# Performance work log

Measured on AMD Instinct MI355X. Metric: run time of the kernel, lower is better.

The kernel has to match this reference:

```python
import jax, jax.numpy as jnp
import numpy as np

N = 10000      # nodes
E = 320000     # edges
F_IN = 33      # input node features
H = 32         # hidden
G = 64         # graphs in batch


def setup_inputs() -> dict:
    key = jax.random.key(0)
    ks = jax.random.split(key, 24)
    s = 0.1  # small init scale for numerical sanity
    inp = {
        "x": jax.random.normal(ks[0], (N, F_IN), jnp.float32),
        "edge_index": jax.random.randint(ks[1], (2, E), 0, N, jnp.int32),
        "edge_attr": jax.random.uniform(ks[2], (E, 1), jnp.float32),
        "batch": jnp.sort(jax.random.randint(ks[3], (N,), 0, G, jnp.int32)),
        # conv1: edge-MLP Linear(1 -> F_IN*H), root weight [F_IN,H], bias [H]
        "nn_w1": jax.random.normal(ks[4], (1, F_IN * H), jnp.float32) * s,
        "nn_b1": jax.random.normal(ks[5], (F_IN * H,), jnp.float32) * s,
        "root1": jax.random.normal(ks[6], (F_IN, H), jnp.float32) * s,
        "bias1": jnp.zeros((H,), jnp.float32),
        # conv2: edge-MLP Linear(1 -> H*H)
        "nn_w2": jax.random.normal(ks[7], (1, H * H), jnp.float32) * s,
        "nn_b2": jax.random.normal(ks[8], (H * H,), jnp.float32) * s,
        "root2": jax.random.normal(ks[9], (H, H), jnp.float32) * s,
        "bias2": jnp.zeros((H,), jnp.float32),
        # conv3
        "nn_w3": jax.random.normal(ks[10], (1, H * H), jnp.float32) * s,
        "nn_b3": jax.random.normal(ks[11], (H * H,), jnp.float32) * s,
        "root3": jax.random.normal(ks[12], (H, H), jnp.float32) * s,
        "bias3": jnp.zeros((H,), jnp.float32),
        # readout MLP: Linear(3H -> H), Linear(H -> 2)
        "lin1_w": jax.random.normal(ks[13], (3 * H, H), jnp.float32) * s,
        "lin1_b": jnp.zeros((H,), jnp.float32),
        "lin2_w": jax.random.normal(ks[14], (H, 2), jnp.float32) * s,
        "lin2_b": jnp.zeros((2,), jnp.float32),
    }
    return inp


def _nnconv(x, src, dst, edge_attr, nn_w, nn_b, root, bias):
    """PyG NNConv (aggr='add'): out_i = x_i @ root + bias + sum_{e: dst(e)=i} x_{src(e)} @ Theta(e_attr)."""
    in_dim, out_dim = root.shape
    # per-edge weight matrix from edge MLP: [E, in, out]
    W = (edge_attr @ nn_w + nn_b).reshape(-1, in_dim, out_dim)
    msg = jnp.einsum('ei,eio->eo', x[src], W)          # gather + per-edge small matmul
    agg = jax.ops.segment_sum(msg, dst, num_segments=N)  # scatter-add into targets
    return agg + x @ root + bias


def reference(x, edge_index, edge_attr, batch,
              nn_w1, nn_b1, root1, bias1,
              nn_w2, nn_b2, root2, bias2,
              nn_w3, nn_b3, root3, bias3,
              lin1_w, lin1_b, lin2_w, lin2_b):
    src, dst = edge_index[0], edge_index[1]
    h = jax.nn.relu(_nnconv(x, src, dst, edge_attr, nn_w1, nn_b1, root1, bias1))
    h = jax.nn.relu(_nnconv(h, src, dst, edge_attr, nn_w2, nn_b2, root2, bias2))
    h = jax.nn.relu(_nnconv(h, src, dst, edge_attr, nn_w3, nn_b3, root3, bias3))
    # global add / mean / max pooling over graphs
    add_p = jax.ops.segment_sum(h, batch, num_segments=G)
    cnt = jax.ops.segment_sum(jnp.ones((N, 1), h.dtype), batch, num_segments=G)
    mean_p = add_p / jnp.maximum(cnt, 1.0)
    max_p = jax.ops.segment_max(h, batch, num_segments=G)
    max_p = jnp.where(jnp.isfinite(max_p), max_p, 0.0)  # guard empty segments
    g = jnp.concatenate([add_p, mean_p, max_p], axis=1)  # [G, 3H]
    g = jax.nn.relu(g @ lin1_w + lin1_b)
    # dropout p=0.5 is identity in eval mode
    logits = g @ lin2_w + lin2_b
    return jax.nn.log_softmax(logits, axis=-1)
```

## Files before the change

### kernel.cpp

```cpp
#include <hip/hip_runtime.h>

constexpr int N_  = 10000;
constexpr int E_  = 320000;
constexpr int F1  = 33;
constexpr int H   = 32;
constexpr int G   = 64;
constexpr int CAP = 96;
constexpr int NB_ = 1280;
constexpr int ROW = CAP * 8;

constexpr int EBLK = E_ / 256;
constexpr int PBLK = N_ / 8;
constexpr int SLICES = 32;
constexpr int CHUNKS = 16;
constexpr int TILE   = 640;
constexpr int AT    = 1024;
constexpr int ITERS = TILE / 128;

__device__ __forceinline__ unsigned bf16r(float x) {
    unsigned u = __float_as_uint(x);
    return (u + 0x7FFFu + ((u >> 16) & 1u)) >> 16;
}

__device__ __forceinline__ size_t mslot(int n, int pos) {
    return (size_t)(n >> 3) * ROW + (size_t)(pos >> 3) * 64 + (n & 7) * 8 + (pos & 7);
}


__global__ __launch_bounds__(256) void k_build_pre1(
        const int* __restrict__ ei, const float* __restrict__ ea,
        const float* __restrict__ x, const int* __restrict__ batch,
        const float* __restrict__ A, const float* __restrict__ Bm,
        const float* __restrict__ Rw, const float* __restrict__ bias,
        int* __restrict__ counts, unsigned* __restrict__ meta2,
        unsigned* __restrict__ UVs, float* __restrict__ Rs,
        int* __restrict__ startsP) {
    __shared__ unsigned s_uv[32][9];
    __shared__ float    s_r[32][9];
    if (blockIdx.x < EBLK) {
        int e = blockIdx.x * 256 + threadIdx.x;
        int s = ei[e];
        int d = ei[E_ + e];
        int pos = atomicAdd(&counts[d], 1);
        meta2[mslot(d, pos)] = (unsigned)s | (bf16r(ea[e]) << 16);
    } else {
        int base8 = (blockIdx.x - EBLK) * 8;
        int grp = threadIdx.x >> 5;
        int f = threadIdx.x & 31;
        int node = base8 + grp;
        if (f == 0) {
            int b = batch[node];
            int bp = (node == 0) ? -1 : batch[node - 1];
            if (b != bp) startsP[b] = node + 1;
        }
        float u = 0.f, v = 0.f, r = bias[f];
        const float* xr = x + (size_t)node * F1;
        #pragma unroll
        for (int k = 0; k < F1; ++k) {
            float xv = xr[k];
            u = fmaf(xv, A[k * H + f], u);
            v = fmaf(xv, Bm[k * H + f], v);
            r = fmaf(xv, Rw[k * H + f], r);
        }
        s_uv[f][grp] = bf16r(u) | (bf16r(v) << 16);
        s_r[f][grp]  = r;
        __syncthreads();
        int fo = threadIdx.x >> 3;
        int nl = threadIdx.x & 7;
        UVs[(size_t)fo * N_ + base8 + nl] = s_uv[fo][nl];
        Rs [(size_t)fo * N_ + base8 + nl] = s_r [fo][nl];
    }
}


__global__ __launch_bounds__(256) void k_pre(
        const float* __restrict__ Hs,
        const float* __restrict__ A, const float* __restrict__ Bm,
        const float* __restrict__ Rw, const float* __restrict__ bias,
        unsigned* __restrict__ UVs, float* __restrict__ Rs) {
    __shared__ unsigned s_uv[32][9];
    __shared__ float    s_r[32][9];
    int base8 = blockIdx.x * 8;
    int grp = threadIdx.x >> 5;
    int f = threadIdx.x & 31;
    int node = base8 + grp;
    float hv = Hs[(size_t)f * N_ + node];
    float u = 0.f, v = 0.f, r = bias[f];
    #pragma unroll
    for (int k = 0; k < H; ++k) {
        float hk = __shfl(hv, k, 32);
        u = fmaf(hk, A[k * H + f], u);
        v = fmaf(hk, Bm[k * H + f], v);
        r = fmaf(hk, Rw[k * H + f], r);
    }
    s_uv[f][grp] = bf16r(u) | (bf16r(v) << 16);
    s_r[f][grp]  = r;
    __syncthreads();
    int fo = threadIdx.x >> 3;
    int nl = threadIdx.x & 7;
    UVs[(size_t)fo * N_ + base8 + nl] = s_uv[fo][nl];
    Rs [(size_t)fo * N_ + base8 + nl] = s_r [fo][nl];
}


__global__ __launch_bounds__(1024, 8) void k_agg_lds(
        const int* __restrict__ counts, const unsigned* __restrict__ meta2,
        const unsigned* __restrict__ UVs, const float* __restrict__ Rs,
        float* __restrict__ Hs) {
    __shared__ __align__(16) unsigned uvl[N_];
    int s     = blockIdx.x & 31;
    int chunk = blockIdx.x >> 5;

    int l   = threadIdx.x & 63;
    int wav = threadIdx.x >> 6;
    int j0  = l & 7;
    int nl  = l >> 3;

    int cbase = chunk * TILE + wav * 8;
    int node = cbase + nl;
    int nc = min(node, N_ - 1);
    int dg = (node < N_) ? counts[nc] : 0;
    float rv = Rs[(size_t)s * N_ + nc];
    const unsigned* mrow = meta2 + (size_t)(cbase >> 3) * ROW + l;
    unsigned m0 = mrow[0], m1 = mrow[64], m2 = mrow[128],
             m3 = mrow[192], m4 = mrow[256], m5 = mrow[320];

    const unsigned* srcp = UVs + (size_t)s * N_;
    #pragma unroll
    for (int i = 0; i < 3; ++i) {
        int d4 = (i * AT + (int)threadIdx.x) * 4;
        if (d4 + 4 <= N_) {
            uint4 t = *reinterpret_cast<const uint4*>(srcp + d4);
            *reinterpret_cast<uint4*>(&uvl[d4]) = t;
        }
    }
    __syncthreads();

    for (int it = 0; it < ITERS; ++it) {
        int nbase = cbase + 128;
        int nnode = nbase + nl;
        int nnc = min(nnode, N_ - 1);
        int ndg = 0; float nrv = 0.f;
        unsigned n0 = 0, n1 = 0, n2 = 0, n3 = 0, n4 = 0, n5 = 0;
        if (it < ITERS - 1) {
            ndg = (nnode < N_) ? counts[nnc] : 0;
            nrv = Rs[(size_t)s * N_ + nnc];
            const unsigned* nmr = meta2 + (size_t)(nbase >> 3) * ROW + l;
            n0 = nmr[0]; n1 = nmr[64]; n2 = nmr[128];
            n3 = nmr[192]; n4 = nmr[256]; n5 = nmr[320];
        }

        float acc = 0.f;
        auto slot = [&](int p, unsigned mv) {
            unsigned idx = min(mv & 0xFFFFu, (unsigned)(N_ - 1));
            unsigned w = uvl[idx];
            float t = fmaf(__uint_as_float(mv & 0xFFFF0000u),
                           __uint_as_float(w << 16),
                           __uint_as_float(w & 0xFFFF0000u));
            if (j0 + 8 * p < dg) acc += t;
        };
        slot(0, m0); slot(1, m1); slot(2, m2);
        slot(3, m3); slot(4, m4); slot(5, m5);
        if (__any(dg > 48)) {
            const unsigned* trow = meta2 + (size_t)(cbase >> 3) * ROW + l;
            for (int p = 6; __any(j0 + 8 * p < dg); ++p)
                slot(p, trow[p * 64]);
        }
        acc += __shfl_xor(acc, 1);
        acc += __shfl_xor(acc, 2);
        acc += __shfl_xor(acc, 4);
        float h = fmaxf(rv + acc, 0.f);
        if (j0 == 0 && node < N_) Hs[(size_t)s * N_ + node] = h;

        cbase = nbase; node = nnode; nc = nnc; dg = ndg; rv = nrv;
        m0 = n0; m1 = n1; m2 = n2; m3 = n3; m4 = n4; m5 = n5;
    }
}


__global__ __launch_bounds__(256) void k_pool(
        const float* __restrict__ Hs, const int* __restrict__ startsP,
        const float* __restrict__ w1, const float* __restrict__ b1,
        const float* __restrict__ w2, const float* __restrict__ b2,
        float* __restrict__ out) {
    __shared__ int sst[G];
    __shared__ float ga[32], gm[32], gx[32];
    int tid = threadIdx.x;
    if (tid < G) sst[tid] = startsP[tid];
    __syncthreads();
    int g = blockIdx.x;
    int sp = sst[g];
    int s = 0, e = 0;
    if (sp != 0) {
        s = sp - 1;
        e = N_;
        for (int j = g + 1; j < G; ++j)
            if (sst[j]) { e = sst[j] - 1; break; }
    }
    int f = tid >> 3, oct = tid & 7;
    float sum = 0.f, mx = 0.f;
    for (int n = s + oct; n < e; n += 8) {
        float w = Hs[(size_t)f * N_ + n];
        sum += w;
        mx = fmaxf(mx, w);
    }
    sum += __shfl_xor(sum, 1); mx = fmaxf(mx, __shfl_xor(mx, 1));
    sum += __shfl_xor(sum, 2); mx = fmaxf(mx, __shfl_xor(mx, 2));
    sum += __shfl_xor(sum, 4); mx = fmaxf(mx, __shfl_xor(mx, 4));
    if (oct == 0) {
        float c = fmaxf((float)(e - s), 1.0f);
        ga[f] = sum;
        gm[f] = sum / c;
        gx[f] = mx;
    }
    __syncthreads();
    if (tid < 32) {
        float hacc = b1[tid];
        #pragma unroll
        for (int k = 0; k < H; ++k) {
            hacc = fmaf(ga[k], w1[k * H + tid], hacc);
            hacc = fmaf(gm[k], w1[(H + k) * H + tid], hacc);
            hacc = fmaf(gx[k], w1[(2 * H + k) * H + tid], hacc);
        }
        float hid = fmaxf(hacc, 0.f);
        float p0 = hid * w2[tid * 2 + 0];
        float p1 = hid * w2[tid * 2 + 1];
        #pragma unroll
        for (int offq = 16; offq; offq >>= 1) {
            p0 += __shfl_xor(p0, offq, 32);
            p1 += __shfl_xor(p1, offq, 32);
        }
        if (tid == 0) {
            float l0 = p0 + b2[0], l1 = p1 + b2[1];
            float m = fmaxf(l0, l1);
            float lse = m + logf(expf(l0 - m) + expf(l1 - m));
            out[g * 2 + 0] = l0 - lse;
            out[g * 2 + 1] = l1 - lse;
        }
    }
}


extern "C" void kernel_launch(void* const* d_in, const int* in_sizes, int n_in,
                              void* d_out, int out_size, void* d_ws, size_t ws_size,
                              hipStream_t stream) {
    const float* x      = (const float*)d_in[0];
    const int*   ei     = (const int*)  d_in[1];
    const float* ea     = (const float*)d_in[2];
    const int*   batch  = (const int*)  d_in[3];
    const float* nn_w1  = (const float*)d_in[4];
    const float* nn_b1  = (const float*)d_in[5];
    const float* root1  = (const float*)d_in[6];
    const float* bias1  = (const float*)d_in[7];
    const float* nn_w2  = (const float*)d_in[8];
    const float* nn_b2  = (const float*)d_in[9];
    const float* root2  = (const float*)d_in[10];
    const float* bias2  = (const float*)d_in[11];
    const float* nn_w3  = (const float*)d_in[12];
    const float* nn_b3  = (const float*)d_in[13];
    const float* root3  = (const float*)d_in[14];
    const float* bias3  = (const float*)d_in[15];
    const float* lin1_w = (const float*)d_in[16];
    const float* lin1_b = (const float*)d_in[17];
    const float* lin2_w = (const float*)d_in[18];
    const float* lin2_b = (const float*)d_in[19];
    float* out = (float*)d_out;

    char* ws = (char*)d_ws;
    size_t off = 0;
    auto alloc = [&](size_t bytes) -> void* {
        void* p = ws + off;
        off += (bytes + 255) & ~(size_t)255;
        return p;
    };
    const size_t zbytes = N_ * sizeof(int) + G * sizeof(int);
    char* zchunk = (char*)alloc(zbytes);
    int*  counts  = (int*)zchunk;
    int*  startsP = (int*)(zchunk + N_ * sizeof(int));
    unsigned* meta2 = (unsigned*)alloc((size_t)NB_ * ROW * sizeof(unsigned));
    unsigned* UVs1 = (unsigned*)alloc((size_t)H * N_ * sizeof(unsigned));
    unsigned* UVs2 = (unsigned*)alloc((size_t)H * N_ * sizeof(unsigned));
    unsigned* UVs3 = (unsigned*)alloc((size_t)H * N_ * sizeof(unsigned));
    float* Rs1 = (float*)alloc((size_t)H * N_ * sizeof(float));
    float* Rs2 = (float*)alloc((size_t)H * N_ * sizeof(float));
    float* Rs3 = (float*)alloc((size_t)H * N_ * sizeof(float));
    float* h1  = (float*)alloc((size_t)H * N_ * sizeof(float));
    float* h2  = (float*)alloc((size_t)H * N_ * sizeof(float));
    float* h3  = (float*)alloc((size_t)H * N_ * sizeof(float));

    hipMemsetAsync(zchunk, 0, zbytes, stream);

    k_build_pre1<<<EBLK + PBLK, 256, 0, stream>>>(ei, ea, x, batch,
                                                  nn_w1, nn_b1, root1, bias1,
                                                  counts, meta2, UVs1, Rs1, startsP);

    k_agg_lds<<<SLICES * CHUNKS, AT, 0, stream>>>(counts, meta2, UVs1, Rs1, h1);
    k_pre    <<<PBLK, 256, 0, stream>>>(h1, nn_w2, nn_b2, root2, bias2, UVs2, Rs2);
    k_agg_lds<<<SLICES * CHUNKS, AT, 0, stream>>>(counts, meta2, UVs2, Rs2, h2);
    k_pre    <<<PBLK, 256, 0, stream>>>(h2, nn_w3, nn_b3, root3, bias3, UVs3, Rs3);
    k_agg_lds<<<SLICES * CHUNKS, AT, 0, stream>>>(counts, meta2, UVs3, Rs3, h3);

    k_pool<<<G, 256, 0, stream>>>(h3, startsP, lin1_w, lin1_b, lin2_w, lin2_b, out);
}
```

Baseline: 169.3 us.

## Fuse all GNN stages into one persistent cooperative kernel with grid syncs

Replaces the memset plus seven separate launches with a single cooperative kernel of 256 blocks of 1024 threads. Grid-wide syncs separate the edge-bucketing, pre-transform, three aggregation and pooling phases, and the counter zeroing moves into the kernel. The aim is to remove launch gaps and tail effects between the small kernels. The cost is fewer blocks per aggregation pass (each block handles two chunks), a reshaped pre/pool work split, grid.sync overheads, and a multi-kernel fallback path if the cooperative launch fails.

```diff
diff --git a/kernel.cpp b/kernel.cpp
--- a/kernel.cpp
+++ b/kernel.cpp
@@ -1,4 +1,7 @@
 #include <hip/hip_runtime.h>
+#include <hip/hip_cooperative_groups.h>
+
+namespace cg = cooperative_groups;
 
 constexpr int N_  = 10000;
 constexpr int E_  = 320000;
@@ -9,13 +12,13 @@
 constexpr int NB_ = 1280;
 constexpr int ROW = CAP * 8;
 
-constexpr int EBLK = E_ / 256;
-constexpr int PBLK = N_ / 8;
+constexpr int GRID   = 256;
+constexpr int BT     = 1024;
 constexpr int SLICES = 32;
 constexpr int CHUNKS = 16;
 constexpr int TILE   = 640;
-constexpr int AT    = 1024;
-constexpr int ITERS = TILE / 128;
+constexpr int ITERS  = TILE / 128;
+constexpr int NG     = 2 * ITERS;
 
 __device__ __forceinline__ unsigned bf16r(float x) {
     unsigned u = __float_as_uint(x);
@@ -26,218 +29,278 @@
     return (size_t)(n >> 3) * ROW + (size_t)(pos >> 3) * 64 + (n & 7) * 8 + (pos & 7);
 }
 
-
-__global__ __launch_bounds__(256) void k_build_pre1(
-        const int* __restrict__ ei, const float* __restrict__ ea,
-        const float* __restrict__ x, const int* __restrict__ batch,
-        const float* __restrict__ A, const float* __restrict__ Bm,
-        const float* __restrict__ Rw, const float* __restrict__ bias,
-        int* __restrict__ counts, unsigned* __restrict__ meta2,
-        unsigned* __restrict__ UVs, float* __restrict__ Rs,
-        int* __restrict__ startsP) {
-    __shared__ unsigned s_uv[32][9];
-    __shared__ float    s_r[32][9];
-    if (blockIdx.x < EBLK) {
-        int e = blockIdx.x * 256 + threadIdx.x;
-        int s = ei[e];
-        int d = ei[E_ + e];
-        int pos = atomicAdd(&counts[d], 1);
-        meta2[mslot(d, pos)] = (unsigned)s | (bf16r(ea[e]) << 16);
-    } else {
-        int base8 = (blockIdx.x - EBLK) * 8;
-        int grp = threadIdx.x >> 5;
-        int f = threadIdx.x & 31;
-        int node = base8 + grp;
-        if (f == 0) {
-            int b = batch[node];
-            int bp = (node == 0) ? -1 : batch[node - 1];
-            if (b != bp) startsP[b] = node + 1;
-        }
-        float u = 0.f, v = 0.f, r = bias[f];
-        const float* xr = x + (size_t)node * F1;
+struct Prm {
+    const float* x; const int* ei; const float* ea; const int* batch;
+    const float* A1; const float* B1; const float* R1; const float* z1;
+    const float* A2; const float* B2; const float* R2; const float* z2;
+    const float* A3; const float* B3; const float* R3; const float* z3;
+    const float* l1w; const float* l1b; const float* l2w; const float* l2b;
+    int* counts; int* startsP; unsigned* meta2;
+    unsigned* UV; float* Rs; float* Hs;
+    float* out;
+};
+
+
+__device__ __forceinline__ void build_phase(const Prm& p, unsigned* uvl) {
+    const int tid = threadIdx.x;
+    const int bid = blockIdx.x;
+
+    for (int e = bid * BT + tid; e < E_; e += GRID * BT) {
+        int s = p.ei[e];
+        int d = p.ei[E_ + e];
+        int pos = atomicAdd(&p.counts[d], 1);
+        p.meta2[mslot(d, pos)] = (unsigned)s | (bf16r(p.ea[e]) << 16);
+    }
+
+    unsigned (*s_uv)[33] = reinterpret_cast<unsigned (*)[33]>(uvl);
+    float    (*s_r )[33] = reinterpret_cast<float (*)[33]>((float*)(uvl + 32 * 33));
+    int grp = tid >> 5, f = tid & 31;
+    for (int t = bid; t * 32 < N_; t += GRID) {
+        int node = t * 32 + grp;
+        int nc = min(node, N_ - 1);
+        if (f == 0 && node < N_) {
+            int b = p.batch[nc];
+            int bp = (node == 0) ? -1 : p.batch[nc - 1];
+            if (b != bp) p.startsP[b] = node + 1;
+        }
+        float u = 0.f, v = 0.f, r = p.z1[f];
+        const float* xr = p.x + (size_t)nc * F1;
         #pragma unroll
         for (int k = 0; k < F1; ++k) {
             float xv = xr[k];
-            u = fmaf(xv, A[k * H + f], u);
-            v = fmaf(xv, Bm[k * H + f], v);
-            r = fmaf(xv, Rw[k * H + f], r);
+            u = fmaf(xv, p.A1[k * H + f], u);
+            v = fmaf(xv, p.B1[k * H + f], v);
+            r = fmaf(xv, p.R1[k * H + f], r);
         }
         s_uv[f][grp] = bf16r(u) | (bf16r(v) << 16);
-        s_r[f][grp]  = r;
+        s_r [f][grp] = r;
         __syncthreads();
-        int fo = threadIdx.x >> 3;
-        int nl = threadIdx.x & 7;
-        UVs[(size_t)fo * N_ + base8 + nl] = s_uv[fo][nl];
-        Rs [(size_t)fo * N_ + base8 + nl] = s_r [fo][nl];
-    }
-}
-
-
-__global__ __launch_bounds__(256) void k_pre(
-        const float* __restrict__ Hs,
+        int fo = tid >> 5, nl = tid & 31;
+        int on = t * 32 + nl;
+        if (on < N_) {
+            p.UV[(size_t)fo * N_ + on] = s_uv[fo][nl];
+            p.Rs[(size_t)fo * N_ + on] = s_r [fo][nl];
+        }
+        __syncthreads();
+    }
+}
+
+
+__device__ __forceinline__ void pre_phase(const Prm& p, unsigned* uvl,
         const float* __restrict__ A, const float* __restrict__ Bm,
-        const float* __restrict__ Rw, const float* __restrict__ bias,
-        unsigned* __restrict__ UVs, float* __restrict__ Rs) {
-    __shared__ unsigned s_uv[32][9];
-    __shared__ float    s_r[32][9];
-    int base8 = blockIdx.x * 8;
-    int grp = threadIdx.x >> 5;
-    int f = threadIdx.x & 31;
-    int node = base8 + grp;
-    float hv = Hs[(size_t)f * N_ + node];
-    float u = 0.f, v = 0.f, r = bias[f];
-    #pragma unroll
-    for (int k = 0; k < H; ++k) {
-        float hk = __shfl(hv, k, 32);
-        u = fmaf(hk, A[k * H + f], u);
-        v = fmaf(hk, Bm[k * H + f], v);
-        r = fmaf(hk, Rw[k * H + f], r);
-    }
-    s_uv[f][grp] = bf16r(u) | (bf16r(v) << 16);
-    s_r[f][grp]  = r;
-    __syncthreads();
-    int fo = threadIdx.x >> 3;
-    int nl = threadIdx.x & 7;
-    UVs[(size_t)fo * N_ + base8 + nl] = s_uv[fo][nl];
-    Rs [(size_t)fo * N_ + base8 + nl] = s_r [fo][nl];
-}
-
-
-__global__ __launch_bounds__(1024, 8) void k_agg_lds(
-        const int* __restrict__ counts, const unsigned* __restrict__ meta2,
-        const unsigned* __restrict__ UVs, const float* __restrict__ Rs,
-        float* __restrict__ Hs) {
-    __shared__ __align__(16) unsigned uvl[N_];
-    int s     = blockIdx.x & 31;
-    int chunk = blockIdx.x >> 5;
-
-    int l   = threadIdx.x & 63;
-    int wav = threadIdx.x >> 6;
-    int j0  = l & 7;
-    int nl  = l >> 3;
-
-    int cbase = chunk * TILE + wav * 8;
+        const float* __restrict__ Rw, const float* __restrict__ bz) {
+    const int tid = threadIdx.x;
+    unsigned (*s_uv)[33] = reinterpret_cast<unsigned (*)[33]>(uvl);
+    float    (*s_r )[33] = reinterpret_cast<float (*)[33]>((float*)(uvl + 32 * 33));
+    int grp = tid >> 5, f = tid & 31;
+    for (int t = blockIdx.x; t * 32 < N_; t += GRID) {
+        int node = t * 32 + grp;
+        int nc = min(node, N_ - 1);
+        float hv = p.Hs[(size_t)f * N_ + nc];
+        float u = 0.f, v = 0.f, r = bz[f];
+        #pragma unroll
+        for (int k = 0; k < H; ++k) {
+            float hk = __shfl(hv, k, 32);
+            u = fmaf(hk, A[k * H + f], u);
+            v = fmaf(hk, Bm[k * H + f], v);
+            r = fmaf(hk, Rw[k * H + f], r);
+        }
+        s_uv[f][grp] = bf16r(u) | (bf16r(v) << 16);
+        s_r [f][grp] = r;
+        __syncthreads();
+        int fo = tid >> 5, nl = tid & 31;
+        int on = t * 32 + nl;
+        if (on < N_) {
+            p.UV[(size_t)fo * N_ + on] = s_uv[fo][nl];
+            p.Rs[(size_t)fo * N_ + on] = s_r [fo][nl];
+        }
+        __syncthreads();
+    }
+}
+
+
+__device__ __forceinline__ void agg_phase(const Prm& p, unsigned* uvl) {
+    const int tid = threadIdx.x;
+    const int s  = blockIdx.x & 31;
+    const int c0 = blockIdx.x >> 5;
+    const int l = tid & 63, wav = tid >> 6, j0 = l & 7, nl = l >> 3;
+
+    auto base_of = [&](int g) {
+        int ch = c0 + ((g >= ITERS) ? 8 : 0);
+        int it = (g >= ITERS) ? (g - ITERS) : g;
+        return ch * TILE + it * 128 + wav * 8;
+    };
+
+    int cbase = base_of(0);
     int node = cbase + nl;
     int nc = min(node, N_ - 1);
-    int dg = (node < N_) ? counts[nc] : 0;
-    float rv = Rs[(size_t)s * N_ + nc];
-    const unsigned* mrow = meta2 + (size_t)(cbase >> 3) * ROW + l;
+    int dg = (node < N_) ? p.counts[nc] : 0;
+    float rv = p.Rs[(size_t)s * N_ + nc];
+    const unsigned* mrow = p.meta2 + (size_t)(cbase >> 3) * ROW + l;
     unsigned m0 = mrow[0], m1 = mrow[64], m2 = mrow[128],
              m3 = mrow[192], m4 = mrow[256], m5 = mrow[320];
 
-    const unsigned* srcp = UVs + (size_t)s * N_;
+    const unsigned* srcp = p.UV + (size_t)s * N_;
     #pragma unroll
     for (int i = 0; i < 3; ++i) {
-        int d4 = (i * AT + (int)threadIdx.x) * 4;
-        if (d4 + 4 <= N_) {
-            uint4 t = *reinterpret_cast<const uint4*>(srcp + d4);
-            *reinterpret_cast<uint4*>(&uvl[d4]) = t;
-        }
+        int d4 = (i * BT + tid) * 4;
+        if (d4 + 4 <= N_)
+            *reinterpret_cast<uint4*>(&uvl[d4]) =
+                *reinterpret_cast<const uint4*>(srcp + d4);
     }
     __syncthreads();
 
-    for (int it = 0; it < ITERS; ++it) {
-        int nbase = cbase + 128;
-        int nnode = nbase + nl;
-        int nnc = min(nnode, N_ - 1);
-        int ndg = 0; float nrv = 0.f;
+    for (int g = 0; g < NG; ++g) {
+        int nbase = 0, nnode = 0, ndg = 0; float nrv = 0.f;
         unsigned n0 = 0, n1 = 0, n2 = 0, n3 = 0, n4 = 0, n5 = 0;
-        if (it < ITERS - 1) {
-            ndg = (nnode < N_) ? counts[nnc] : 0;
-            nrv = Rs[(size_t)s * N_ + nnc];
-            const unsigned* nmr = meta2 + (size_t)(nbase >> 3) * ROW + l;
+        if (g + 1 < NG) {
+            nbase = base_of(g + 1);
+            nnode = nbase + nl;
+            int nnc = min(nnode, N_ - 1);
+            ndg = (nnode < N_) ? p.counts[nnc] : 0;
+            nrv = p.Rs[(size_t)s * N_ + nnc];
+            const unsigned* nmr = p.meta2 + (size_t)(nbase >> 3) * ROW + l;
             n0 = nmr[0]; n1 = nmr[64]; n2 = nmr[128];
             n3 = nmr[192]; n4 = nmr[256]; n5 = nmr[320];
         }
 
         float acc = 0.f;
-        auto slot = [&](int p, unsigned mv) {
+        auto slot = [&](unsigned mv, int pq) {
             unsigned idx = min(mv & 0xFFFFu, (unsigned)(N_ - 1));
             unsigned w = uvl[idx];
             float t = fmaf(__uint_as_float(mv & 0xFFFF0000u),
                            __uint_as_float(w << 16),
                            __uint_as_float(w & 0xFFFF0000u));
-            if (j0 + 8 * p < dg) acc += t;
+            if (j0 + 8 * pq < dg) acc += t;
         };
-        slot(0, m0); slot(1, m1); slot(2, m2);
-        slot(3, m3); slot(4, m4); slot(5, m5);
+        slot(m0, 0); slot(m1, 1); slot(m2, 2);
+        slot(m3, 3); slot(m4, 4); slot(m5, 5);
         if (__any(dg > 48)) {
-            const unsigned* trow = meta2 + (size_t)(cbase >> 3) * ROW + l;
-            for (int p = 6; __any(j0 + 8 * p < dg); ++p)
-                slot(p, trow[p * 64]);
+            const unsigned* trow = p.meta2 + (size_t)(cbase >> 3) * ROW + l;
+            for (int pq = 6; __any(j0 + 8 * pq < dg); ++pq)
+                slot(trow[pq * 64], pq);
         }
         acc += __shfl_xor(acc, 1);
         acc += __shfl_xor(acc, 2);
         acc += __shfl_xor(acc, 4);
         float h = fmaxf(rv + acc, 0.f);
-        if (j0 == 0 && node < N_) Hs[(size_t)s * N_ + node] = h;
-
-        cbase = nbase; node = nnode; nc = nnc; dg = ndg; rv = nrv;
+        if (j0 == 0 && node < N_) p.Hs[(size_t)s * N_ + node] = h;
+
+        cbase = nbase; node = nnode; dg = ndg; rv = nrv;
         m0 = n0; m1 = n1; m2 = n2; m3 = n3; m4 = n4; m5 = n5;
     }
 }
 
 
-__global__ __launch_bounds__(256) void k_pool(
-        const float* __restrict__ Hs, const int* __restrict__ startsP,
-        const float* __restrict__ w1, const float* __restrict__ b1,
-        const float* __restrict__ w2, const float* __restrict__ b2,
-        float* __restrict__ out) {
-    __shared__ int sst[G];
-    __shared__ float ga[32], gm[32], gx[32];
-    int tid = threadIdx.x;
-    if (tid < G) sst[tid] = startsP[tid];
+__device__ __forceinline__ void pool_phase(const Prm& p, int* sst, float* gpl) {
+    const int tid = threadIdx.x;
+    int g = blockIdx.x;
+    if (tid < G) sst[tid] = p.startsP[tid];
     __syncthreads();
-    int g = blockIdx.x;
     int sp = sst[g];
-    int s = 0, e = 0;
+    int s0 = 0, e0 = 0;
     if (sp != 0) {
-        s = sp - 1;
-        e = N_;
+        s0 = sp - 1;
+        e0 = N_;
         for (int j = g + 1; j < G; ++j)
-            if (sst[j]) { e = sst[j] - 1; break; }
-    }
-    int f = tid >> 3, oct = tid & 7;
+            if (sst[j]) { e0 = sst[j] - 1; break; }
+    }
+    int f = tid >> 5, oct = tid & 31;
     float sum = 0.f, mx = 0.f;
-    for (int n = s + oct; n < e; n += 8) {
-        float w = Hs[(size_t)f * N_ + n];
+    for (int n = s0 + oct; n < e0; n += 32) {
+        float w = p.Hs[(size_t)f * N_ + n];
         sum += w;
         mx = fmaxf(mx, w);
     }
-    sum += __shfl_xor(sum, 1); mx = fmaxf(mx, __shfl_xor(mx, 1));
-    sum += __shfl_xor(sum, 2); mx = fmaxf(mx, __shfl_xor(mx, 2));
-    sum += __shfl_xor(sum, 4); mx = fmaxf(mx, __shfl_xor(mx, 4));
+    #pragma unroll
+    for (int o = 1; o <= 16; o <<= 1) {
+        sum += __shfl_xor(sum, o);
+        mx = fmaxf(mx, __shfl_xor(mx, o));
+    }
     if (oct == 0) {
-        float c = fmaxf((float)(e - s), 1.0f);
-        ga[f] = sum;
-        gm[f] = sum / c;
-        gx[f] = mx;
+        float c = fmaxf((float)(e0 - s0), 1.0f);
+        gpl[f] = sum;
+        gpl[H + f] = sum / c;
+        gpl[2 * H + f] = mx;
     }
     __syncthreads();
     if (tid < 32) {
-        float hacc = b1[tid];
+        float hacc = p.l1b[tid];
         #pragma unroll
         for (int k = 0; k < H; ++k) {
-            hacc = fmaf(ga[k], w1[k * H + tid], hacc);
-            hacc = fmaf(gm[k], w1[(H + k) * H + tid], hacc);
-            hacc = fmaf(gx[k], w1[(2 * H + k) * H + tid], hacc);
+            hacc = fmaf(gpl[k],         p.l1w[k * H + tid], hacc);
+            hacc = fmaf(gpl[H + k],     p.l1w[(H + k) * H + tid], hacc);
+            hacc = fmaf(gpl[2 * H + k], p.l1w[(2 * H + k) * H + tid], hacc);
         }
         float hid = fmaxf(hacc, 0.f);
-        float p0 = hid * w2[tid * 2 + 0];
-        float p1 = hid * w2[tid * 2 + 1];
+        float p0 = hid * p.l2w[tid * 2 + 0];
+        float p1 = hid * p.l2w[tid * 2 + 1];
         #pragma unroll
-        for (int offq = 16; offq; offq >>= 1) {
-            p0 += __shfl_xor(p0, offq, 32);
-            p1 += __shfl_xor(p1, offq, 32);
+        for (int o = 16; o; o >>= 1) {
+            p0 += __shfl_xor(p0, o, 32);
+            p1 += __shfl_xor(p1, o, 32);
         }
         if (tid == 0) {
-            float l0 = p0 + b2[0], l1 = p1 + b2[1];
+            float l0 = p0 + p.l2b[0], l1 = p1 + p.l2b[1];
             float m = fmaxf(l0, l1);
             float lse = m + logf(expf(l0 - m) + expf(l1 - m));
-            out[g * 2 + 0] = l0 - lse;
-            out[g * 2 + 1] = l1 - lse;
-        }
-    }
+            p.out[g * 2 + 0] = l0 - lse;
+            p.out[g * 2 + 1] = l1 - lse;
+        }
+    }
+}
+
+
+__global__ __launch_bounds__(BT, 4) void k_fused(Prm p) {
+    cg::grid_group grid = cg::this_grid();
+    __shared__ __align__(16) unsigned uvl[N_];
+    __shared__ int   sst[G];
+    __shared__ float gpl[3 * H];
+    const int tid = threadIdx.x;
+    const int bid = blockIdx.x;
+
+    {
+        int i = bid * BT + tid;
+        if (i < N_) p.counts[i] = 0;
+        else if (i < N_ + G) p.startsP[i - N_] = 0;
+    }
+    grid.sync();
+
+    build_phase(p, uvl);
+    grid.sync();
+
+    agg_phase(p, uvl);
+    grid.sync();
+    pre_phase(p, uvl, p.A2, p.B2, p.R2, p.z2);
+    grid.sync();
+    agg_phase(p, uvl);
+    grid.sync();
+    pre_phase(p, uvl, p.A3, p.B3, p.R3, p.z3);
+    grid.sync();
+    agg_phase(p, uvl);
+    grid.sync();
+
+    if (bid < G) pool_phase(p, sst, gpl);
+}
+
+
+__global__ __launch_bounds__(BT, 4) void kf_build(Prm p) {
+    __shared__ __align__(16) unsigned uvl[N_];
+    build_phase(p, uvl);
+}
+__global__ __launch_bounds__(BT, 4) void kf_agg(Prm p) {
+    __shared__ __align__(16) unsigned uvl[N_];
+    agg_phase(p, uvl);
+}
+__global__ __launch_bounds__(BT, 4) void kf_pre(Prm p, int layer) {
+    __shared__ __align__(16) unsigned uvl[N_];
+    if (layer == 2) pre_phase(p, uvl, p.A2, p.B2, p.R2, p.z2);
+    else            pre_phase(p, uvl, p.A3, p.B3, p.R3, p.z3);
+}
+__global__ __launch_bounds__(BT, 4) void kf_pool(Prm p) {
+    __shared__ int   sst[G];
+    __shared__ float gpl[3 * H];
+    pool_phase(p, sst, gpl);
 }
 
 
@@ -278,27 +341,29 @@
     int*  counts  = (int*)zchunk;
     int*  startsP = (int*)(zchunk + N_ * sizeof(int));
     unsigned* meta2 = (unsigned*)alloc((size_t)NB_ * ROW * sizeof(unsigned));
-    unsigned* UVs1 = (unsigned*)alloc((size_t)H * N_ * sizeof(unsigned));
-    unsigned* UVs2 = (unsigned*)alloc((size_t)H * N_ * sizeof(unsigned));
-    unsigned* UVs3 = (unsigned*)alloc((size_t)H * N_ * sizeof(unsigned));
-    float* Rs1 = (float*)alloc((size_t)H * N_ * sizeof(float));
-    float* Rs2 = (float*)alloc((size_t)H * N_ * sizeof(float));
-    float* Rs3 = (float*)alloc((size_t)H * N_ * sizeof(float));
-    float* h1  = (float*)alloc((size_t)H * N_ * sizeof(float));
-    float* h2  = (float*)alloc((size_t)H * N_ * sizeof(float));
-    float* h3  = (float*)alloc((size_t)H * N_ * sizeof(float));
-
-    hipMemsetAsync(zchunk, 0, zbytes, stream);
-
-    k_build_pre1<<<EBLK + PBLK, 256, 0, stream>>>(ei, ea, x, batch,
-                                                  nn_w1, nn_b1, root1, bias1,
-                                                  counts, meta2, UVs1, Rs1, startsP);
-
-    k_agg_lds<<<SLICES * CHUNKS, AT, 0, stream>>>(counts, meta2, UVs1, Rs1, h1);
-    k_pre    <<<PBLK, 256, 0, stream>>>(h1, nn_w2, nn_b2, root2, bias2, UVs2, Rs2);
-    k_agg_lds<<<SLICES * CHUNKS, AT, 0, stream>>>(counts, meta2, UVs2, Rs2, h2);
-    k_pre    <<<PBLK, 256, 0, stream>>>(h2, nn_w3, nn_b3, root3, bias3, UVs3, Rs3);
-    k_agg_lds<<<SLICES * CHUNKS, AT, 0, stream>>>(counts, meta2, UVs3, Rs3, h3);
-
-    k_pool<<<G, 256, 0, stream>>>(h3, startsP, lin1_w, lin1_b, lin2_w, lin2_b, out);
-}
+    unsigned* UV = (unsigned*)alloc((size_t)H * N_ * sizeof(unsigned));
+    float*    Rs = (float*)   alloc((size_t)H * N_ * sizeof(float));
+    float*    Hs = (float*)   alloc((size_t)H * N_ * sizeof(float));
+
+    Prm prm{ x, ei, ea, batch,
+             nn_w1, nn_b1, root1, bias1,
+             nn_w2, nn_b2, root2, bias2,
+             nn_w3, nn_b3, root3, bias3,
+             lin1_w, lin1_b, lin2_w, lin2_b,
+             counts, startsP, meta2, UV, Rs, Hs, out };
+
+    void* args[] = { &prm };
+    hipError_t err = hipLaunchCooperativeKernel((const void*)k_fused,
+                                                dim3(GRID), dim3(BT),
+                                                args, 0, stream);
+    if (err != hipSuccess) {
+        hipMemsetAsync(zchunk, 0, zbytes, stream);
+        kf_build<<<GRID, BT, 0, stream>>>(prm);
+        kf_agg  <<<GRID, BT, 0, stream>>>(prm);
+        kf_pre  <<<GRID, BT, 0, stream>>>(prm, 2);
+        kf_agg  <<<GRID, BT, 0, stream>>>(prm);
+        kf_pre  <<<GRID, BT, 0, stream>>>(prm, 3);
+        kf_agg  <<<GRID, BT, 0, stream>>>(prm);
+        kf_pool <<<G, BT, 0, stream>>>(prm);
+    }
+}
```

Measured after the change: 397.5 us. 2.35x slower.
